# Kernel tuning notes

Hardware: AMD Instinct MI355X
Metric: run time of the kernel (lower is better)

## Reference

```python
import jax, jax.numpy as jnp
import numpy as np

# Quantization constants (from init_kwargs)
INPUT_SCALE = 0.05
OUTPUT_SCALE = 0.1
OUTPUT_ZERO_POINT = 0
FEATURE_BITWIDTH = 8
Q_MIN = -(1 << (FEATURE_BITWIDTH - 1))       # -128
Q_MAX = (1 << (FEATURE_BITWIDTH - 1)) - 1    #  127

B, IN_F, OUT_F = 8192, 4096, 4096


def setup_inputs() -> dict:
    key = jax.random.key(0)
    k_x, k_w, k_b, k_s = jax.random.split(key, 4)
    # int8 quantized activations and weights
    x = jax.random.randint(k_x, (B, IN_F), Q_MIN, Q_MAX + 1, dtype=jnp.int8)
    weight = jax.random.randint(k_w, (OUT_F, IN_F), Q_MIN, Q_MAX + 1, dtype=jnp.int8)
    # shifted quantized bias (int32)
    bias = jax.random.randint(k_b, (OUT_F,), -1000, 1000, dtype=jnp.int32)
    # per-output-channel weight scale (positive floats)
    weight_scale = jax.random.uniform(k_s, (OUT_F,), dtype=jnp.float32, minval=0.001, maxval=0.01)
    return {"x": x, "weight": weight, "bias": bias, "weight_scale": weight_scale}


def reference(x, weight, bias, weight_scale):
    # int32-accumulated GEMM: [B, in] @ [in, out] + bias -> [B, out]
    acc = jnp.matmul(x.astype(jnp.int32), weight.astype(jnp.int32).T,
                     preferred_element_type=jnp.int32) + bias[None, :]
    # dequant/requant epilogue with per-channel scale
    out = acc.astype(jnp.float32) * (INPUT_SCALE * weight_scale[None, :] / OUTPUT_SCALE) + OUTPUT_ZERO_POINT
    out = jnp.clip(jnp.round(out), Q_MIN, Q_MAX).astype(jnp.int8)
    return out
```

## Files before the change

kernel.cpp:

```cpp
#include <hip/hip_runtime.h>
#include <cstdint>
#include <cstddef>

#define M_DIM 8192
#define N_DIM 4096
#define K_DIM 4096

#define BM 128
#define BN 128
#define BK 64

using i32x4 = __attribute__((ext_vector_type(4))) int;

__device__ __forceinline__ void async_load16(const void* g, void* l) {
    __builtin_amdgcn_global_load_lds(
        (const __attribute__((address_space(1))) void*)g,
        (__attribute__((address_space(3))) void*)l,
        16, 0, 0);
}

__global__ __launch_bounds__(256) void pack_i8_kernel(const int4* __restrict__ xsrc,
                                                      int* __restrict__ xdst,
                                                      const int4* __restrict__ wsrc,
                                                      int* __restrict__ wdst,
                                                      int nxblocks) {
    const bool isw = (int)blockIdx.x >= nxblocks;
    const int4* src = isw ? wsrc : xsrc;
    int*       dst  = isw ? wdst : xdst;
    const long bb   = isw ? ((long)blockIdx.x - nxblocks) : (long)blockIdx.x;
    const long base = bb * 1024 + threadIdx.x;
#pragma unroll
    for (int j = 0; j < 4; ++j) {
        const long i = base + 256 * j;
        const int4 v = src[i];
        dst[i] = (v.x & 0xff) | ((v.y & 0xff) << 8) | ((v.z & 0xff) << 16) | (v.w << 24);
    }
}

__global__ __launch_bounds__(256) void qgemm_i8_kernel(const int8_t* __restrict__ A,
                                                       const int8_t* __restrict__ B,
                                                       const int* __restrict__ bias,
                                                       const float* __restrict__ wscale,
                                                       int* __restrict__ C) {
    __shared__ int8_t As[2][BM * BK];
    __shared__ int8_t Bs[2][BN * BK];

    const int tid  = threadIdx.x;
    const int wave = tid >> 6;
    const int lane = tid & 63;
    const int bm = blockIdx.y;
    const int bn = blockIdx.x;

    const int8_t* Ab = A + (size_t)bm * BM * K_DIM;
    const int8_t* Bb = B + (size_t)bn * BN * K_DIM;

    const int wm = wave >> 1;
    const int wn = wave & 1;

    i32x4 acc[4][4] = {};

    const int srow = lane >> 2;
    const int scol = (lane & 3) * 16;

    const int kq   = (lane >> 4) * 16;
    const int mrow = wm * 64 + (lane & 15);
    const int nrow = wn * 64 + (lane & 15);

#pragma unroll
    for (int c = 0; c < 2; ++c) {
        const int rbase = (c * 4 + wave) * 16;
        async_load16(Ab + (size_t)(rbase + srow) * K_DIM + 0 + scol,
                     &As[0][(c * 4 + wave) * 1024]);
        async_load16(Bb + (size_t)(rbase + srow) * K_DIM + 0 + scol,
                     &Bs[0][(c * 4 + wave) * 1024]);
    }
    __syncthreads();

    int cur = 0;
    for (int kt = 0; kt < K_DIM; kt += BK) {
        if (kt + BK < K_DIM) {
#pragma unroll
            for (int c = 0; c < 2; ++c) {
                const int rbase = (c * 4 + wave) * 16;
                async_load16(Ab + (size_t)(rbase + srow) * K_DIM + (kt + BK) + scol,
                             &As[cur ^ 1][(c * 4 + wave) * 1024]);
                async_load16(Bb + (size_t)(rbase + srow) * K_DIM + (kt + BK) + scol,
                             &Bs[cur ^ 1][(c * 4 + wave) * 1024]);
            }
        }

        i32x4 af[4], bf[4];
#pragma unroll
        for (int i = 0; i < 4; ++i)
            af[i] = *(const i32x4*)&As[cur][(mrow + i * 16) * BK + kq];
#pragma unroll
        for (int j = 0; j < 4; ++j)
            bf[j] = *(const i32x4*)&Bs[cur][(nrow + j * 16) * BK + kq];

#pragma unroll
        for (int i = 0; i < 4; ++i)
#pragma unroll
            for (int j = 0; j < 4; ++j)
                acc[i][j] = __builtin_amdgcn_mfma_i32_16x16x64_i8(af[i], bf[j], acc[i][j], 0, 0, 0);

        __syncthreads();
        cur ^= 1;
    }

    const int col16 = lane & 15;
    const int rquad = (lane >> 4) * 4;
#pragma unroll
    for (int j = 0; j < 4; ++j) {
        const int col = bn * BN + wn * 64 + j * 16 + col16;
        float s = 0.05f * wscale[col];
        s = s / 0.1f;
        const float bz = (float)bias[col];
#pragma unroll
        for (int i = 0; i < 4; ++i) {
            const int row0 = bm * BM + wm * 64 + i * 16 + rquad;
#pragma unroll
            for (int r = 0; r < 4; ++r) {
                float v = ((float)acc[i][j][r] + bz) * s;
                v = rintf(v);
                v = fminf(fmaxf(v, -128.0f), 127.0f);
                C[(size_t)(row0 + r) * N_DIM + col] = (int)v;
            }
        }
    }
}

extern "C" void kernel_launch(void* const* d_in, const int* in_sizes, int n_in,
                              void* d_out, int out_size, void* d_ws, size_t ws_size,
                              hipStream_t stream) {
    const int*   x32    = (const int*)d_in[0];
    const int*   w32    = (const int*)d_in[1];
    const int*   bias   = (const int*)d_in[2];
    const float* wscale = (const float*)d_in[3];
    int*         out    = (int*)d_out;

    int8_t* xp = (int8_t*)d_ws;
    int8_t* wp = xp + (size_t)M_DIM * K_DIM;

    {
        const int nxblocks = (int)((long)M_DIM * K_DIM / 4 / 1024);
        const int nwblocks = (int)((long)N_DIM * K_DIM / 4 / 1024);
        pack_i8_kernel<<<nxblocks + nwblocks, 256, 0, stream>>>(
            (const int4*)x32, (int*)xp, (const int4*)w32, (int*)wp, nxblocks);
    }

    dim3 grid(N_DIM / BN, M_DIM / BM);
    qgemm_i8_kernel<<<grid, 256, 0, stream>>>(xp, wp, bias, wscale, out);
}
```

Baseline: 437.2 us.

## Rewrite int8 GEMM as 256x256 tile, 8-wave, ping-pong pipelined MFMA kernel

Replaces the 128x128x64 double-buffered GEMM with a 256x256 tile using 512 threads and BK=128. LDS is XOR-swizzled to avoid bank conflicts, and loads are split into half-tiles issued across eight phases with explicit vmcnt waits, barriers and setprio around MFMA bursts. The aim is more data reuse per block and better overlap of global-to-LDS copies with matrix math. In exchange it uses 128KB of LDS per block and relies on fragile hand-tuned waitcnt and scheduling.

```diff
diff --git a/kernel.cpp b/kernel.cpp
--- a/kernel.cpp
+++ b/kernel.cpp
@@ -6,9 +6,8 @@
 #define N_DIM 4096
 #define K_DIM 4096
 
-#define BM 128
-#define BN 128
-#define BK 64
+#define BM 256
+#define BN 256
 
 using i32x4 = __attribute__((ext_vector_type(4))) int;
 
@@ -37,93 +36,129 @@
     }
 }
 
-__global__ __launch_bounds__(256) void qgemm_i8_kernel(const int8_t* __restrict__ A,
-                                                       const int8_t* __restrict__ B,
-                                                       const int* __restrict__ bias,
-                                                       const float* __restrict__ wscale,
-                                                       int* __restrict__ C) {
-    __shared__ int8_t As[2][BM * BK];
-    __shared__ int8_t Bs[2][BN * BK];
+__global__ __launch_bounds__(512, 2) void qgemm_i8_kernel(const int8_t* __restrict__ A,
+                                                          const int8_t* __restrict__ B,
+                                                          const int* __restrict__ bias,
+                                                          const float* __restrict__ wscale,
+                                                          int* __restrict__ C) {
+    __shared__ int8_t LDS[131072];
 
     const int tid  = threadIdx.x;
     const int wave = tid >> 6;
     const int lane = tid & 63;
+    const int wm = wave >> 2;
+    const int wn = wave & 3;
     const int bm = blockIdx.y;
     const int bn = blockIdx.x;
 
     const int8_t* Ab = A + (size_t)bm * BM * K_DIM;
     const int8_t* Bb = B + (size_t)bn * BN * K_DIM;
 
-    const int wm = wave >> 1;
-    const int wn = wave & 1;
+    const int l8 = lane >> 3;
+    const int l7 = lane & 7;
+    const int8_t* Ag = Ab + (size_t)(wave * 16 + l8) * K_DIM + ((l7 ^ l8) * 16);
+    const int8_t* Bg = Bb + (size_t)(wave * 16 + l8) * K_DIM + ((l7 ^ l8) * 16);
+    const int sdst = wave * 2048;
 
-    i32x4 acc[4][4] = {};
+    const int l15 = lane & 15;
+    const int qh  = lane >> 4;
+    const int a_off0 = wm * 8192 + l15 * 128 + ((qh ^ l7) * 16);
+    const int a_off1 = a_off0 ^ 64;
+    const int b_off0 = 65536 + wn * 4096 + l15 * 128 + ((qh ^ l7) * 16);
+    const int b_off1 = b_off0 ^ 64;
 
-    const int srow = lane >> 2;
-    const int scol = (lane & 3) * 16;
+    i32x4 acc[4][4][2] = {};
 
-    const int kq   = (lane >> 4) * 16;
-    const int mrow = wm * 64 + (lane & 15);
-    const int nrow = wn * 64 + (lane & 15);
+#define ISSUE_HT(GB, REG, BUF, HH, T) do { \
+    async_load16((GB) + (size_t)((HH) * 128)     * K_DIM + (size_t)(T) * 128, \
+                 &LDS[(REG) + (BUF) * 32768 + (HH) * 16384 + sdst]); \
+    async_load16((GB) + (size_t)((HH) * 128 + 8) * K_DIM + (size_t)(T) * 128, \
+                 &LDS[(REG) + (BUF) * 32768 + (HH) * 16384 + sdst + 1024]); \
+} while (0)
 
-#pragma unroll
-    for (int c = 0; c < 2; ++c) {
-        const int rbase = (c * 4 + wave) * 16;
-        async_load16(Ab + (size_t)(rbase + srow) * K_DIM + 0 + scol,
-                     &As[0][(c * 4 + wave) * 1024]);
-        async_load16(Bb + (size_t)(rbase + srow) * K_DIM + 0 + scol,
-                     &Bs[0][(c * 4 + wave) * 1024]);
+#define PHASE(BUF, MH, NH, QD, ISSUES, CHK) do { \
+    i32x4 af[4][2]; i32x4 bf[2][2]; \
+    _Pragma("unroll") \
+    for (int mi = 0; mi < 4; ++mi) { \
+        af[mi][0] = *(const i32x4*)&LDS[a_off0 + (BUF) * 32768 + (MH) * 16384 + mi * 2048]; \
+        af[mi][1] = *(const i32x4*)&LDS[a_off1 + (BUF) * 32768 + (MH) * 16384 + mi * 2048]; \
+    } \
+    _Pragma("unroll") \
+    for (int ni = 0; ni < 2; ++ni) { \
+        bf[ni][0] = *(const i32x4*)&LDS[b_off0 + (BUF) * 32768 + (NH) * 16384 + ni * 2048]; \
+        bf[ni][1] = *(const i32x4*)&LDS[b_off1 + (BUF) * 32768 + (NH) * 16384 + ni * 2048]; \
+    } \
+    ISSUES; \
+    CHK; \
+    __builtin_amdgcn_s_barrier(); \
+    asm volatile("s_waitcnt lgkmcnt(0)" ::: "memory"); \
+    __builtin_amdgcn_sched_barrier(0); \
+    __builtin_amdgcn_s_setprio(1); \
+    _Pragma("unroll") \
+    for (int mi = 0; mi < 4; ++mi) { \
+        _Pragma("unroll") \
+        for (int ni = 0; ni < 2; ++ni) { \
+            acc[QD][mi][ni] = __builtin_amdgcn_mfma_i32_16x16x64_i8(af[mi][0], bf[ni][0], acc[QD][mi][ni], 0, 0, 0); \
+            acc[QD][mi][ni] = __builtin_amdgcn_mfma_i32_16x16x64_i8(af[mi][1], bf[ni][1], acc[QD][mi][ni], 0, 0, 0); \
+        } \
+    } \
+    __builtin_amdgcn_s_setprio(0); \
+    __builtin_amdgcn_s_barrier(); \
+} while (0)
+
+    ISSUE_HT(Bg, 65536, 0, 0, 0);
+    ISSUE_HT(Ag, 0,     0, 1, 0);
+    ISSUE_HT(Ag, 0,     0, 0, 0);
+    ISSUE_HT(Bg, 65536, 0, 1, 0);
+    ISSUE_HT(Bg, 65536, 1, 0, 1);
+    ISSUE_HT(Ag, 0,     1, 1, 1);
+    asm volatile("s_waitcnt vmcnt(4)" ::: "memory");
+    __builtin_amdgcn_s_barrier();
+
+    for (int i = 0; i < 16; ++i) {
+        const int V = 2 * i + 1;
+        const int W = 2 * i + 2;
+        const int X = 2 * i + 3;
+        const bool more = (i < 15);
+
+        PHASE(0, 0, 0, 0, { ISSUE_HT(Ag, 0,     1, 0, V); }, {});
+        PHASE(0, 1, 0, 1, { ISSUE_HT(Bg, 65536, 1, 1, V); }, {});
+        PHASE(0, 1, 1, 2, { if (more) ISSUE_HT(Bg, 65536, 0, 0, W); }, {});
+        PHASE(0, 0, 1, 3, { if (more) ISSUE_HT(Ag, 0,     0, 1, W); },
+              { if (more) { asm volatile("s_waitcnt vmcnt(4)" ::: "memory"); }
+                else      { asm volatile("s_waitcnt vmcnt(0)" ::: "memory"); } });
+        PHASE(1, 0, 0, 0, { if (more) ISSUE_HT(Ag, 0,     0, 0, W); }, {});
+        PHASE(1, 1, 0, 1, { if (more) ISSUE_HT(Bg, 65536, 0, 1, W); }, {});
+        PHASE(1, 1, 1, 2, { if (more) ISSUE_HT(Bg, 65536, 1, 0, X); }, {});
+        PHASE(1, 0, 1, 3, { if (more) ISSUE_HT(Ag, 0,     1, 1, X); },
+              { if (more) { asm volatile("s_waitcnt vmcnt(4)" ::: "memory"); } });
     }
-    __syncthreads();
 
-    int cur = 0;
-    for (int kt = 0; kt < K_DIM; kt += BK) {
-        if (kt + BK < K_DIM) {
-#pragma unroll
-            for (int c = 0; c < 2; ++c) {
-                const int rbase = (c * 4 + wave) * 16;
-                async_load16(Ab + (size_t)(rbase + srow) * K_DIM + (kt + BK) + scol,
-                             &As[cur ^ 1][(c * 4 + wave) * 1024]);
-                async_load16(Bb + (size_t)(rbase + srow) * K_DIM + (kt + BK) + scol,
-                             &Bs[cur ^ 1][(c * 4 + wave) * 1024]);
-            }
-        }
-
-        i32x4 af[4], bf[4];
-#pragma unroll
-        for (int i = 0; i < 4; ++i)
-            af[i] = *(const i32x4*)&As[cur][(mrow + i * 16) * BK + kq];
-#pragma unroll
-        for (int j = 0; j < 4; ++j)
-            bf[j] = *(const i32x4*)&Bs[cur][(nrow + j * 16) * BK + kq];
-
-#pragma unroll
-        for (int i = 0; i < 4; ++i)
-#pragma unroll
-            for (int j = 0; j < 4; ++j)
-                acc[i][j] = __builtin_amdgcn_mfma_i32_16x16x64_i8(af[i], bf[j], acc[i][j], 0, 0, 0);
-
-        __syncthreads();
-        cur ^= 1;
-    }
+#undef PHASE
+#undef ISSUE_HT
 
     const int col16 = lane & 15;
     const int rquad = (lane >> 4) * 4;
 #pragma unroll
-    for (int j = 0; j < 4; ++j) {
-        const int col = bn * BN + wn * 64 + j * 16 + col16;
-        float s = 0.05f * wscale[col];
-        s = s / 0.1f;
-        const float bz = (float)bias[col];
+    for (int qd = 0; qd < 4; ++qd) {
+        const int mh = (qd & 1) ^ (qd >> 1);
+        const int nh = qd >> 1;
 #pragma unroll
-        for (int i = 0; i < 4; ++i) {
-            const int row0 = bm * BM + wm * 64 + i * 16 + rquad;
+        for (int ni = 0; ni < 2; ++ni) {
+            const int col = bn * BN + nh * 128 + wn * 32 + ni * 16 + col16;
+            float s = 0.05f * wscale[col];
+            s = s / 0.1f;
+            const float bz = (float)bias[col];
 #pragma unroll
-            for (int r = 0; r < 4; ++r) {
-                float v = ((float)acc[i][j][r] + bz) * s;
-                v = rintf(v);
-                v = fminf(fmaxf(v, -128.0f), 127.0f);
-                C[(size_t)(row0 + r) * N_DIM + col] = (int)v;
+            for (int mi = 0; mi < 4; ++mi) {
+                const int row0 = bm * BM + mh * 128 + wm * 64 + mi * 16 + rquad;
+#pragma unroll
+                for (int r = 0; r < 4; ++r) {
+                    float v = ((float)acc[qd][mi][ni][r] + bz) * s;
+                    v = rintf(v);
+                    v = fminf(fmaxf(v, -128.0f), 127.0f);
+                    C[(size_t)(row0 + r) * N_DIM + col] = (int)v;
+                }
             }
         }
     }
@@ -149,5 +184,5 @@
     }
 
     dim3 grid(N_DIM / BN, M_DIM / BM);
-    qgemm_i8_kernel<<<grid, 256, 0, stream>>>(xp, wp, bias, wscale, out);
+    qgemm_i8_kernel<<<grid, 512, 0, stream>>>(xp, wp, bias, wscale, out);
 }
```

Result: faster. 407.4 us (-6.8%).
